# Optimization experiments

Measured on AMD Instinct MI355X. Metric: run time of the kernel, lower is better.

## Reference

```python
import jax, jax.numpy as jnp
import numpy as np

N = 50000   # nodes
E = 800000  # edges (avg degree 16)
IN, H, OUT = 128, 128, 64


def setup_inputs() -> dict:
    key = jax.random.key(0)
    ks = jax.random.split(key, 8)

    def w(k, shape):
        fan_in = shape[0]
        return (jax.random.normal(k, shape, jnp.float32) / np.float32(np.sqrt(fan_in)))

    x = jax.random.normal(ks[0], (N, IN), jnp.float32)
    edge_index = jax.random.randint(ks[1], (2, E), 0, N, jnp.int64)
    return {
        "x": x,
        "edge_index": edge_index,
        "W1": w(ks[2], (IN, H)), "b1": jnp.zeros((H,), jnp.float32),
        "W2": w(ks[3], (H, H)),  "b2": jnp.zeros((H,), jnp.float32),
        "W3": w(ks[4], (H, H)),  "b3": jnp.zeros((H,), jnp.float32),
        "Wd1": w(ks[5], (H, H)), "bd1": jnp.zeros((H,), jnp.float32),
        "Wd2": w(ks[6], (H, OUT)), "bd2": jnp.zeros((OUT,), jnp.float32),
    }


def _gcn_conv(x, src, dst, norm, W, b):
    # x: [N, Cin] -> linear transform, gather along edges, normalized scatter-add
    h = x @ W                                   # [N, Cout]
    msg = h[src] * norm[:, None]                # [E+N, Cout]
    out = jax.ops.segment_sum(msg, dst, num_segments=N)
    return out + b


def reference(x, edge_index, W1, b1, W2, b2, W3, b3, Wd1, bd1, Wd2, bd2):
    # Add self-loops (PyG GCNConv default) and compute symmetric normalization.
    loops = jnp.arange(N, dtype=edge_index.dtype)
    src = jnp.concatenate([edge_index[0], loops])   # [E+N]
    dst = jnp.concatenate([edge_index[1], loops])   # [E+N]
    deg = jax.ops.segment_sum(jnp.ones_like(dst, dtype=x.dtype), dst, num_segments=N)
    dinv = jnp.where(deg > 0, jax.lax.rsqrt(deg), jnp.zeros_like(deg))
    norm = dinv[src] * dinv[dst]                    # [E+N]

    h = jax.nn.relu(_gcn_conv(x, src, dst, norm, W1, b1))
    h = jax.nn.relu(_gcn_conv(h, src, dst, norm, W2, b2))
    h = jax.nn.relu(_gcn_conv(h, src, dst, norm, W3, b3))

    h = jax.nn.relu(h @ Wd1 + bd1)
    return jax.nn.sigmoid(h @ Wd2 + bd2)            # [N, OUT]
```

## Files before the change

kernel.cpp:

```cpp
#include <hip/hip_runtime.h>
#include <hip/hip_bf16.h>
#include <hip/hip_fp16.h>

#define N_NODES 50000
#define N_EDGES 800000
#define C_H 128
#define C_OUT 64
#define NBLK 196
#define TSTRIDE 136
#define E_PAD 950272

typedef __attribute__((ext_vector_type(8))) short bf16x8;
typedef __attribute__((ext_vector_type(4))) float f32x4;

static __device__ __forceinline__ float bf_lo(unsigned int u) { return __uint_as_float(u << 16); }
static __device__ __forceinline__ float bf_hi(unsigned int u) { return __uint_as_float(u & 0xffff0000u); }
static __device__ __forceinline__ unsigned short f2bf(float f) {
    __hip_bfloat16 h = __float2bfloat16(f);
    return *(unsigned short*)&h;
}
static __device__ __forceinline__ unsigned int pack2(float a, float b) {
    return (unsigned int)f2bf(a) | ((unsigned int)f2bf(b) << 16);
}
static __device__ __forceinline__ unsigned short f2h_bits(float f) {
    union { __half h; unsigned short u; } c; c.h = __float2half_rn(f); return c.u;
}
static __device__ __forceinline__ float h_bits2f(unsigned short u) {
    union { __half h; unsigned short u; } c; c.u = u; return __half2float(c.h);
}

__global__ void prep_kernel(const float* __restrict__ x, unsigned short* __restrict__ xb,
                            const int* __restrict__ dst, int* __restrict__ counts,
                            const float* __restrict__ W1, const float* __restrict__ W2,
                            const float* __restrict__ W3, const float* __restrict__ Wd1,
                            const float* __restrict__ Wd2,
                            unsigned short* __restrict__ P1, unsigned short* __restrict__ P2,
                            unsigned short* __restrict__ P3, unsigned short* __restrict__ Pd1,
                            unsigned short* __restrict__ Pd2) {
    int b = blockIdx.x;
    if (b < 6250) {
        int i = b * 256 + threadIdx.x;
        float4 v = *(const float4*)(x + (size_t)i * 4);
        ushort4 u;
        u.x = f2bf(v.x); u.y = f2bf(v.y); u.z = f2bf(v.z); u.w = f2bf(v.w);
        *(ushort4*)(xb + (size_t)i * 4) = u;
    } else if (b < 6250 + 3125) {
        int e = (b - 6250) * 256 + threadIdx.x;
        atomicAdd(&counts[dst[e]], 1);
    } else {
        int idx = (b - 9375) * 256 + threadIdx.x;
        if (idx < 4 * 16384) {
            int which = idx >> 14;
            int r = idx & 16383;
            const float* W = (which == 0) ? W1 : (which == 1) ? W2 : (which == 2) ? W3 : Wd1;
            unsigned short* P = (which == 0) ? P1 : (which == 1) ? P2 : (which == 2) ? P3 : Pd1;
            int j = r & 7, lane = (r >> 3) & 63, t = r >> 9;
            int nb = t & 7, kb = t >> 3;
            int k = kb * 32 + ((lane >> 4) << 3) + j;
            int n = nb * 16 + (lane & 15);
            P[r] = f2bf(W[(size_t)k * 128 + n]);
        } else {
            int r = idx - 65536;
            if (r < 8192) {
                int j = r & 7, lane = (r >> 3) & 63, t = r >> 9;
                int nb = t & 3, kb = t >> 2;
                int k = kb * 32 + ((lane >> 4) << 3) + j;
                int n = nb * 16 + (lane & 15);
                Pd2[r] = f2bf(Wd2[(size_t)k * 64 + n]);
            }
        }
    }
}

__global__ void __launch_bounds__(256) scan1_kernel(const int* __restrict__ counts,
                                                    int* __restrict__ eblk,
                                                    int* __restrict__ bsum,
                                                    float* __restrict__ dinv) {
    __shared__ int ws[4];
    int i = blockIdx.x * 256 + threadIdx.x;
    int v = (i < N_NODES) ? counts[i] : 0;
    if (i < N_NODES) dinv[i] = rsqrtf((float)v + 1.0f);
    int vp = (v + 3) & ~3;
    int lane = threadIdx.x & 63, w = threadIdx.x >> 6;
    int x = vp;
    #pragma unroll
    for (int off = 1; off < 64; off <<= 1) {
        int t = __shfl_up(x, off, 64);
        if (lane >= off) x += t;
    }
    if (lane == 63) ws[w] = x;
    __syncthreads();
    if (threadIdx.x == 0) {
        int run = 0;
        #pragma unroll
        for (int k = 0; k < 4; ++k) { int t = ws[k]; ws[k] = run; run += t; }
        bsum[blockIdx.x] = run;
    }
    __syncthreads();
    if (i < N_NODES) eblk[i] = x - vp + ws[w];
}

__global__ void __launch_bounds__(256) scan2_kernel(const int* __restrict__ bsum,
                                                    int* __restrict__ bo,
                                                    int* __restrict__ rowptr) {
    __shared__ int ws[4];
    int i = threadIdx.x;
    int v = (i < NBLK) ? bsum[i] : 0;
    int lane = i & 63, w = i >> 6;
    int x = v;
    #pragma unroll
    for (int off = 1; off < 64; off <<= 1) {
        int t = __shfl_up(x, off, 64);
        if (lane >= off) x += t;
    }
    if (lane == 63) ws[w] = x;
    __syncthreads();
    if (i == 0) {
        int run = 0;
        #pragma unroll
        for (int k = 0; k < 4; ++k) { int t = ws[k]; ws[k] = run; run += t; }
    }
    __syncthreads();
    int excl = x - v + ws[w];
    if (i < NBLK) bo[i] = excl;
    if (i == 255) rowptr[N_NODES] = excl + v;
}

__global__ void scan3_kernel(const int* __restrict__ eblk, const int* __restrict__ bo,
                             int* __restrict__ rowptr, int* __restrict__ cursor) {
    int i = blockIdx.x * 256 + threadIdx.x;
    if (i < N_NODES) {
        int r = eblk[i] + bo[blockIdx.x];
        rowptr[i] = r;
        cursor[i] = r;
    }
}

__global__ void csr_fill_kernel(const int* __restrict__ src, const int* __restrict__ dst,
                                const float* __restrict__ dinv,
                                int* __restrict__ cursor,
                                unsigned int* __restrict__ epay) {
    int e = blockIdx.x * 256 + threadIdx.x;
    if (e < N_EDGES) {
        int d = dst[e], s = src[e];
        int pos = atomicAdd(&cursor[d], 1);
        float nrm = dinv[s] * dinv[d];
        epay[pos] = (unsigned int)s | ((unsigned int)f2h_bits(nrm) << 16);
    }
}

template <bool FINAL>
__global__ void __launch_bounds__(256) fused_layer_kernel(
        const int* __restrict__ rowptr,
        const unsigned int* __restrict__ epay,
        const float* __restrict__ dinv,
        const unsigned short* __restrict__ hin,
        const unsigned short* __restrict__ Wp,
        const float* __restrict__ bias,
        const unsigned short* __restrict__ Wd1p,
        const float* __restrict__ bd1,
        const unsigned short* __restrict__ Wd2p,
        const float* __restrict__ bd2,
        unsigned short* __restrict__ out_b,
        float* __restrict__ out_f) {
    __shared__ unsigned short sG[16 * TSTRIDE];
    const int t = threadIdx.x;

    {
        int nl = t >> 4, c8 = (t & 15) << 3;
        int node = blockIdx.x * 16 + nl;
        float di = dinv[node], dii = di * di;
        uint4 raw = *(const uint4*)(hin + (size_t)node * C_H + c8);
        float a0 = bf_lo(raw.x) * dii, a1 = bf_hi(raw.x) * dii;
        float a2 = bf_lo(raw.y) * dii, a3 = bf_hi(raw.y) * dii;
        float a4 = bf_lo(raw.z) * dii, a5 = bf_hi(raw.z) * dii;
        float a6 = bf_lo(raw.w) * dii, a7 = bf_hi(raw.w) * dii;
        int beg = rowptr[node], end = rowptr[node + 1];
        for (int p = beg; p < end; p += 4) {
            uint4 ev = *(const uint4*)(epay + p);
            int   s0 = (int)(ev.x & 0xffffu); float n0 = h_bits2f((unsigned short)(ev.x >> 16));
            int   s1 = (int)(ev.y & 0xffffu); float n1 = h_bits2f((unsigned short)(ev.y >> 16));
            int   s2 = (int)(ev.z & 0xffffu); float n2 = h_bits2f((unsigned short)(ev.z >> 16));
            int   s3 = (int)(ev.w & 0xffffu); float n3 = h_bits2f((unsigned short)(ev.w >> 16));
            uint4 r0 = *(const uint4*)(hin + (size_t)s0 * C_H + c8);
            uint4 r1 = *(const uint4*)(hin + (size_t)s1 * C_H + c8);
            uint4 r2 = *(const uint4*)(hin + (size_t)s2 * C_H + c8);
            uint4 r3 = *(const uint4*)(hin + (size_t)s3 * C_H + c8);
            a0 = fmaf(bf_lo(r0.x), n0, a0); a1 = fmaf(bf_hi(r0.x), n0, a1);
            a2 = fmaf(bf_lo(r0.y), n0, a2); a3 = fmaf(bf_hi(r0.y), n0, a3);
            a4 = fmaf(bf_lo(r0.z), n0, a4); a5 = fmaf(bf_hi(r0.z), n0, a5);
            a6 = fmaf(bf_lo(r0.w), n0, a6); a7 = fmaf(bf_hi(r0.w), n0, a7);
            a0 = fmaf(bf_lo(r1.x), n1, a0); a1 = fmaf(bf_hi(r1.x), n1, a1);
            a2 = fmaf(bf_lo(r1.y), n1, a2); a3 = fmaf(bf_hi(r1.y), n1, a3);
            a4 = fmaf(bf_lo(r1.z), n1, a4); a5 = fmaf(bf_hi(r1.z), n1, a5);
            a6 = fmaf(bf_lo(r1.w), n1, a6); a7 = fmaf(bf_hi(r1.w), n1, a7);
            a0 = fmaf(bf_lo(r2.x), n2, a0); a1 = fmaf(bf_hi(r2.x), n2, a1);
            a2 = fmaf(bf_lo(r2.y), n2, a2); a3 = fmaf(bf_hi(r2.y), n2, a3);
            a4 = fmaf(bf_lo(r2.z), n2, a4); a5 = fmaf(bf_hi(r2.z), n2, a5);
            a6 = fmaf(bf_lo(r2.w), n2, a6); a7 = fmaf(bf_hi(r2.w), n2, a7);
            a0 = fmaf(bf_lo(r3.x), n3, a0); a1 = fmaf(bf_hi(r3.x), n3, a1);
            a2 = fmaf(bf_lo(r3.y), n3, a2); a3 = fmaf(bf_hi(r3.y), n3, a3);
            a4 = fmaf(bf_lo(r3.z), n3, a4); a5 = fmaf(bf_hi(r3.z), n3, a5);
            a6 = fmaf(bf_lo(r3.w), n3, a6); a7 = fmaf(bf_hi(r3.w), n3, a7);
        }
        uint4 o;
        o.x = pack2(a0, a1); o.y = pack2(a2, a3);
        o.z = pack2(a4, a5); o.w = pack2(a6, a7);
        *(uint4*)(sG + nl * TSTRIDE + c8) = o;
    }
    __syncthreads();

    const int lane = t & 63, wave = t >> 6, quad = lane >> 4, row = lane & 15;
    const int node = blockIdx.x * 16 + row;

    f32x4 acc0 = (f32x4){0.f, 0.f, 0.f, 0.f};
    f32x4 acc1 = (f32x4){0.f, 0.f, 0.f, 0.f};
    const int nb0 = 2 * wave, nb1 = 2 * wave + 1;
    #pragma unroll
    for (int kb = 0; kb < 4; ++kb) {
        bf16x8 hf = *(const bf16x8*)(sG + row * TSTRIDE + kb * 32 + quad * 8);
        bf16x8 wf0 = *(const bf16x8*)(Wp + ((size_t)(kb * 8 + nb0) * 64 + lane) * 8);
        bf16x8 wf1 = *(const bf16x8*)(Wp + ((size_t)(kb * 8 + nb1) * 64 + lane) * 8);
        acc0 = __builtin_amdgcn_mfma_f32_16x16x32_bf16(wf0, hf, acc0, 0, 0, 0);
        acc1 = __builtin_amdgcn_mfma_f32_16x16x32_bf16(wf1, hf, acc1, 0, 0, 0);
    }
    float4 ba0 = *(const float4*)(bias + nb0 * 16 + quad * 4);
    float4 ba1 = *(const float4*)(bias + nb1 * 16 + quad * 4);
    float v00 = fmaxf(acc0[0] + ba0.x, 0.f), v01 = fmaxf(acc0[1] + ba0.y, 0.f);
    float v02 = fmaxf(acc0[2] + ba0.z, 0.f), v03 = fmaxf(acc0[3] + ba0.w, 0.f);
    float v10 = fmaxf(acc1[0] + ba1.x, 0.f), v11 = fmaxf(acc1[1] + ba1.y, 0.f);
    float v12 = fmaxf(acc1[2] + ba1.z, 0.f), v13 = fmaxf(acc1[3] + ba1.w, 0.f);

    if (!FINAL) {
        uint2 o0, o1;
        o0.x = pack2(v00, v01); o0.y = pack2(v02, v03);
        o1.x = pack2(v10, v11); o1.y = pack2(v12, v13);
        *(uint2*)(out_b + (size_t)node * C_H + nb0 * 16 + quad * 4) = o0;
        *(uint2*)(out_b + (size_t)node * C_H + nb1 * 16 + quad * 4) = o1;
        return;
    }

    __syncthreads();
    {
        uint2 o0, o1;
        o0.x = pack2(v00, v01); o0.y = pack2(v02, v03);
        o1.x = pack2(v10, v11); o1.y = pack2(v12, v13);
        *(uint2*)(sG + row * TSTRIDE + nb0 * 16 + quad * 4) = o0;
        *(uint2*)(sG + row * TSTRIDE + nb1 * 16 + quad * 4) = o1;
    }
    __syncthreads();

    acc0 = (f32x4){0.f, 0.f, 0.f, 0.f};
    acc1 = (f32x4){0.f, 0.f, 0.f, 0.f};
    #pragma unroll
    for (int kb = 0; kb < 4; ++kb) {
        bf16x8 hf = *(const bf16x8*)(sG + row * TSTRIDE + kb * 32 + quad * 8);
        bf16x8 wf0 = *(const bf16x8*)(Wd1p + ((size_t)(kb * 8 + nb0) * 64 + lane) * 8);
        bf16x8 wf1 = *(const bf16x8*)(Wd1p + ((size_t)(kb * 8 + nb1) * 64 + lane) * 8);
        acc0 = __builtin_amdgcn_mfma_f32_16x16x32_bf16(wf0, hf, acc0, 0, 0, 0);
        acc1 = __builtin_amdgcn_mfma_f32_16x16x32_bf16(wf1, hf, acc1, 0, 0, 0);
    }
    ba0 = *(const float4*)(bd1 + nb0 * 16 + quad * 4);
    ba1 = *(const float4*)(bd1 + nb1 * 16 + quad * 4);
    v00 = fmaxf(acc0[0] + ba0.x, 0.f); v01 = fmaxf(acc0[1] + ba0.y, 0.f);
    v02 = fmaxf(acc0[2] + ba0.z, 0.f); v03 = fmaxf(acc0[3] + ba0.w, 0.f);
    v10 = fmaxf(acc1[0] + ba1.x, 0.f); v11 = fmaxf(acc1[1] + ba1.y, 0.f);
    v12 = fmaxf(acc1[2] + ba1.z, 0.f); v13 = fmaxf(acc1[3] + ba1.w, 0.f);
    __syncthreads();
    {
        uint2 o0, o1;
        o0.x = pack2(v00, v01); o0.y = pack2(v02, v03);
        o1.x = pack2(v10, v11); o1.y = pack2(v12, v13);
        *(uint2*)(sG + row * TSTRIDE + nb0 * 16 + quad * 4) = o0;
        *(uint2*)(sG + row * TSTRIDE + nb1 * 16 + quad * 4) = o1;
    }
    __syncthreads();

    f32x4 acc = (f32x4){0.f, 0.f, 0.f, 0.f};
    #pragma unroll
    for (int kb = 0; kb < 4; ++kb) {
        bf16x8 hf = *(const bf16x8*)(sG + row * TSTRIDE + kb * 32 + quad * 8);
        bf16x8 wf = *(const bf16x8*)(Wd2p + ((size_t)(kb * 4 + wave) * 64 + lane) * 8);
        acc = __builtin_amdgcn_mfma_f32_16x16x32_bf16(wf, hf, acc, 0, 0, 0);
    }
    int ch = wave * 16 + quad * 4;
    float4 b4 = *(const float4*)(bd2 + ch);
    float4 r;
    r.x = 1.f / (1.f + expf(-(acc[0] + b4.x)));
    r.y = 1.f / (1.f + expf(-(acc[1] + b4.y)));
    r.z = 1.f / (1.f + expf(-(acc[2] + b4.z)));
    r.w = 1.f / (1.f + expf(-(acc[3] + b4.w)));
    *(float4*)(out_f + (size_t)node * C_OUT + ch) = r;
}

extern "C" void kernel_launch(void* const* d_in, const int* in_sizes, int n_in,
                              void* d_out, int out_size, void* d_ws, size_t ws_size,
                              hipStream_t stream) {
    const float* x   = (const float*)d_in[0];
    const int*   ei  = (const int*)d_in[1];
    const float* W1  = (const float*)d_in[2];
    const float* b1  = (const float*)d_in[3];
    const float* W2  = (const float*)d_in[4];
    const float* b2  = (const float*)d_in[5];
    const float* W3  = (const float*)d_in[6];
    const float* b3  = (const float*)d_in[7];
    const float* Wd1 = (const float*)d_in[8];
    const float* bd1 = (const float*)d_in[9];
    const float* Wd2 = (const float*)d_in[10];
    const float* bd2 = (const float*)d_in[11];

    const int* src = ei;
    const int* dst = ei + N_EDGES;

    char* base = (char*)d_ws;
    size_t off = 0;
    auto alloc = [&](size_t bytes) { char* p = base + off; off += (bytes + 255) & ~size_t(255); return p; };
    int*            counts = (int*)alloc(50176 * 4);
    unsigned int*   epay   = (unsigned int*)alloc((size_t)E_PAD * 4);
    float*          dinv   = (float*)alloc(N_NODES * 4);
    int*            rowptr = (int*)alloc((N_NODES + 1) * 4);
    int*            cursor = (int*)alloc(N_NODES * 4);
    int*            eblk   = (int*)alloc(N_NODES * 4);
    int*            bsum   = (int*)alloc(256 * 4);
    int*            bo     = (int*)alloc(256 * 4);
    unsigned short* xb     = (unsigned short*)alloc((size_t)N_NODES * C_H * 2);
    unsigned short* bufA   = (unsigned short*)alloc((size_t)N_NODES * C_H * 2);
    unsigned short* bufB   = (unsigned short*)alloc((size_t)N_NODES * C_H * 2);
    unsigned short* P1     = (unsigned short*)alloc(128 * 128 * 2);
    unsigned short* P2     = (unsigned short*)alloc(128 * 128 * 2);
    unsigned short* P3     = (unsigned short*)alloc(128 * 128 * 2);
    unsigned short* Pd1    = (unsigned short*)alloc(128 * 128 * 2);
    unsigned short* Pd2    = (unsigned short*)alloc(128 * 64 * 2);

    const int T = 256;
    dim3 blk(T);
    dim3 gN((N_NODES + T - 1) / T);
    dim3 gE((N_EDGES + T - 1) / T);
    dim3 gPrep(6250 + 3125 + 288);
    dim3 gFused(N_NODES / 16);

    hipMemsetAsync(counts, 0, 50176 * 4 + (size_t)E_PAD * 4, stream);
    prep_kernel<<<gPrep, blk, 0, stream>>>(x, xb, dst, counts,
                                           W1, W2, W3, Wd1, Wd2, P1, P2, P3, Pd1, Pd2);
    scan1_kernel<<<gN, blk, 0, stream>>>(counts, eblk, bsum, dinv);
    scan2_kernel<<<1, blk, 0, stream>>>(bsum, bo, rowptr);
    scan3_kernel<<<gN, blk, 0, stream>>>(eblk, bo, rowptr, cursor);
    csr_fill_kernel<<<gE, blk, 0, stream>>>(src, dst, dinv, cursor, epay);

    fused_layer_kernel<false><<<gFused, blk, 0, stream>>>(
        rowptr, epay, dinv, xb, P1, b1, nullptr, nullptr, nullptr, nullptr, bufA, nullptr);
    fused_layer_kernel<false><<<gFused, blk, 0, stream>>>(
        rowptr, epay, dinv, bufA, P2, b2, nullptr, nullptr, nullptr, nullptr, bufB, nullptr);
    fused_layer_kernel<true><<<gFused, blk, 0, stream>>>(
        rowptr, epay, dinv, bufB, P3, b3, Pd1, bd1, Pd2, bd2, nullptr, (float*)d_out);
}
```

Measured before the change: 280.9 us.

## Record edge ranks during counting, drop cursor atomics, widen gather unroll

The degree-counting pass now stores the return value of its atomicAdd as a per-edge rank. The CSR fill then computes each slot as rowptr[dst] + rank, with no second pass of atomics on a cursor array. Zeroing of the padded edge payload moves from the memset into extra prep blocks. The gather loop now processes 8 edges per iteration, issuing eight independent row loads before the FMAs for more memory-level parallelism, with a 4-edge tail step. The cost is an extra 3.2 MB rank array written and read, plus higher register pressure in the fused layer kernel.

```diff
diff --git a/kernel.cpp b/kernel.cpp
--- a/kernel.cpp
+++ b/kernel.cpp
@@ -31,12 +31,14 @@
 
 __global__ void prep_kernel(const float* __restrict__ x, unsigned short* __restrict__ xb,
                             const int* __restrict__ dst, int* __restrict__ counts,
+                            int* __restrict__ rank,
                             const float* __restrict__ W1, const float* __restrict__ W2,
                             const float* __restrict__ W3, const float* __restrict__ Wd1,
                             const float* __restrict__ Wd2,
                             unsigned short* __restrict__ P1, unsigned short* __restrict__ P2,
                             unsigned short* __restrict__ P3, unsigned short* __restrict__ Pd1,
-                            unsigned short* __restrict__ Pd2) {
+                            unsigned short* __restrict__ Pd2,
+                            unsigned int* __restrict__ epay) {
     int b = blockIdx.x;
     if (b < 6250) {
         int i = b * 256 + threadIdx.x;
@@ -44,10 +46,10 @@
         ushort4 u;
         u.x = f2bf(v.x); u.y = f2bf(v.y); u.z = f2bf(v.z); u.w = f2bf(v.w);
         *(ushort4*)(xb + (size_t)i * 4) = u;
-    } else if (b < 6250 + 3125) {
+    } else if (b < 9375) {
         int e = (b - 6250) * 256 + threadIdx.x;
-        atomicAdd(&counts[dst[e]], 1);
-    } else {
+        rank[e] = atomicAdd(&counts[dst[e]], 1);
+    } else if (b < 9663) {
         int idx = (b - 9375) * 256 + threadIdx.x;
         if (idx < 4 * 16384) {
             int which = idx >> 14;
@@ -69,6 +71,9 @@
                 Pd2[r] = f2bf(Wd2[(size_t)k * 64 + n]);
             }
         }
+    } else {
+        int i = (b - 9663) * 256 + threadIdx.x;
+        *(uint4*)(epay + (size_t)i * 4) = make_uint4(0, 0, 0, 0);
     }
 }
 
@@ -127,23 +132,19 @@
 }
 
 __global__ void scan3_kernel(const int* __restrict__ eblk, const int* __restrict__ bo,
-                             int* __restrict__ rowptr, int* __restrict__ cursor) {
+                             int* __restrict__ rowptr) {
     int i = blockIdx.x * 256 + threadIdx.x;
-    if (i < N_NODES) {
-        int r = eblk[i] + bo[blockIdx.x];
-        rowptr[i] = r;
-        cursor[i] = r;
-    }
+    if (i < N_NODES) rowptr[i] = eblk[i] + bo[blockIdx.x];
 }
 
 __global__ void csr_fill_kernel(const int* __restrict__ src, const int* __restrict__ dst,
                                 const float* __restrict__ dinv,
-                                int* __restrict__ cursor,
+                                const int* __restrict__ rowptr, const int* __restrict__ rank,
                                 unsigned int* __restrict__ epay) {
     int e = blockIdx.x * 256 + threadIdx.x;
     if (e < N_EDGES) {
         int d = dst[e], s = src[e];
-        int pos = atomicAdd(&cursor[d], 1);
+        int pos = rowptr[d] + rank[e];
         float nrm = dinv[s] * dinv[d];
         epay[pos] = (unsigned int)s | ((unsigned int)f2h_bits(nrm) << 16);
     }
@@ -176,32 +177,39 @@
         float a4 = bf_lo(raw.z) * dii, a5 = bf_hi(raw.z) * dii;
         float a6 = bf_lo(raw.w) * dii, a7 = bf_hi(raw.w) * dii;
         int beg = rowptr[node], end = rowptr[node + 1];
-        for (int p = beg; p < end; p += 4) {
+        int p = beg;
+        for (; p + 8 <= end; p += 8) {
+            uint4 ev0 = *(const uint4*)(epay + p);
+            uint4 ev1 = *(const uint4*)(epay + p + 4);
+            unsigned int ee[8] = {ev0.x, ev0.y, ev0.z, ev0.w, ev1.x, ev1.y, ev1.z, ev1.w};
+            uint4 rv[8];
+            #pragma unroll
+            for (int j = 0; j < 8; ++j)
+                rv[j] = *(const uint4*)(hin + (size_t)(ee[j] & 0xffffu) * C_H + c8);
+            #pragma unroll
+            for (int j = 0; j < 8; ++j) {
+                float nm = h_bits2f((unsigned short)(ee[j] >> 16));
+                a0 = fmaf(bf_lo(rv[j].x), nm, a0); a1 = fmaf(bf_hi(rv[j].x), nm, a1);
+                a2 = fmaf(bf_lo(rv[j].y), nm, a2); a3 = fmaf(bf_hi(rv[j].y), nm, a3);
+                a4 = fmaf(bf_lo(rv[j].z), nm, a4); a5 = fmaf(bf_hi(rv[j].z), nm, a5);
+                a6 = fmaf(bf_lo(rv[j].w), nm, a6); a7 = fmaf(bf_hi(rv[j].w), nm, a7);
+            }
+        }
+        if (p < end) {
             uint4 ev = *(const uint4*)(epay + p);
-            int   s0 = (int)(ev.x & 0xffffu); float n0 = h_bits2f((unsigned short)(ev.x >> 16));
-            int   s1 = (int)(ev.y & 0xffffu); float n1 = h_bits2f((unsigned short)(ev.y >> 16));
-            int   s2 = (int)(ev.z & 0xffffu); float n2 = h_bits2f((unsigned short)(ev.z >> 16));
-            int   s3 = (int)(ev.w & 0xffffu); float n3 = h_bits2f((unsigned short)(ev.w >> 16));
-            uint4 r0 = *(const uint4*)(hin + (size_t)s0 * C_H + c8);
-            uint4 r1 = *(const uint4*)(hin + (size_t)s1 * C_H + c8);
-            uint4 r2 = *(const uint4*)(hin + (size_t)s2 * C_H + c8);
-            uint4 r3 = *(const uint4*)(hin + (size_t)s3 * C_H + c8);
-            a0 = fmaf(bf_lo(r0.x), n0, a0); a1 = fmaf(bf_hi(r0.x), n0, a1);
-            a2 = fmaf(bf_lo(r0.y), n0, a2); a3 = fmaf(bf_hi(r0.y), n0, a3);
-            a4 = fmaf(bf_lo(r0.z), n0, a4); a5 = fmaf(bf_hi(r0.z), n0, a5);
-            a6 = fmaf(bf_lo(r0.w), n0, a6); a7 = fmaf(bf_hi(r0.w), n0, a7);
-            a0 = fmaf(bf_lo(r1.x), n1, a0); a1 = fmaf(bf_hi(r1.x), n1, a1);
-            a2 = fmaf(bf_lo(r1.y), n1, a2); a3 = fmaf(bf_hi(r1.y), n1, a3);
-            a4 = fmaf(bf_lo(r1.z), n1, a4); a5 = fmaf(bf_hi(r1.z), n1, a5);
-            a6 = fmaf(bf_lo(r1.w), n1, a6); a7 = fmaf(bf_hi(r1.w), n1, a7);
-            a0 = fmaf(bf_lo(r2.x), n2, a0); a1 = fmaf(bf_hi(r2.x), n2, a1);
-            a2 = fmaf(bf_lo(r2.y), n2, a2); a3 = fmaf(bf_hi(r2.y), n2, a3);
-            a4 = fmaf(bf_lo(r2.z), n2, a4); a5 = fmaf(bf_hi(r2.z), n2, a5);
-            a6 = fmaf(bf_lo(r2.w), n2, a6); a7 = fmaf(bf_hi(r2.w), n2, a7);
-            a0 = fmaf(bf_lo(r3.x), n3, a0); a1 = fmaf(bf_hi(r3.x), n3, a1);
-            a2 = fmaf(bf_lo(r3.y), n3, a2); a3 = fmaf(bf_hi(r3.y), n3, a3);
-            a4 = fmaf(bf_lo(r3.z), n3, a4); a5 = fmaf(bf_hi(r3.z), n3, a5);
-            a6 = fmaf(bf_lo(r3.w), n3, a6); a7 = fmaf(bf_hi(r3.w), n3, a7);
+            unsigned int ee[4] = {ev.x, ev.y, ev.z, ev.w};
+            uint4 rv[4];
+            #pragma unroll
+            for (int j = 0; j < 4; ++j)
+                rv[j] = *(const uint4*)(hin + (size_t)(ee[j] & 0xffffu) * C_H + c8);
+            #pragma unroll
+            for (int j = 0; j < 4; ++j) {
+                float nm = h_bits2f((unsigned short)(ee[j] >> 16));
+                a0 = fmaf(bf_lo(rv[j].x), nm, a0); a1 = fmaf(bf_hi(rv[j].x), nm, a1);
+                a2 = fmaf(bf_lo(rv[j].y), nm, a2); a3 = fmaf(bf_hi(rv[j].y), nm, a3);
+                a4 = fmaf(bf_lo(rv[j].z), nm, a4); a5 = fmaf(bf_hi(rv[j].z), nm, a5);
+                a6 = fmaf(bf_lo(rv[j].w), nm, a6); a7 = fmaf(bf_hi(rv[j].w), nm, a7);
+            }
         }
         uint4 o;
         o.x = pack2(a0, a1); o.y = pack2(a2, a3);
@@ -317,9 +325,9 @@
     auto alloc = [&](size_t bytes) { char* p = base + off; off += (bytes + 255) & ~size_t(255); return p; };
     int*            counts = (int*)alloc(50176 * 4);
     unsigned int*   epay   = (unsigned int*)alloc((size_t)E_PAD * 4);
+    int*            rank   = (int*)alloc((size_t)N_EDGES * 4);
     float*          dinv   = (float*)alloc(N_NODES * 4);
     int*            rowptr = (int*)alloc((N_NODES + 1) * 4);
-    int*            cursor = (int*)alloc(N_NODES * 4);
     int*            eblk   = (int*)alloc(N_NODES * 4);
     int*            bsum   = (int*)alloc(256 * 4);
     int*            bo     = (int*)alloc(256 * 4);
@@ -336,16 +344,17 @@
     dim3 blk(T);
     dim3 gN((N_NODES + T - 1) / T);
     dim3 gE((N_EDGES + T - 1) / T);
-    dim3 gPrep(6250 + 3125 + 288);
+    dim3 gPrep(6250 + 3125 + 288 + 928);
     dim3 gFused(N_NODES / 16);
 
-    hipMemsetAsync(counts, 0, 50176 * 4 + (size_t)E_PAD * 4, stream);
-    prep_kernel<<<gPrep, blk, 0, stream>>>(x, xb, dst, counts,
-                                           W1, W2, W3, Wd1, Wd2, P1, P2, P3, Pd1, Pd2);
+    hipMemsetAsync(counts, 0, 50176 * 4, stream);
+    prep_kernel<<<gPrep, blk, 0, stream>>>(x, xb, dst, counts, rank,
+                                           W1, W2, W3, Wd1, Wd2,
+                                           P1, P2, P3, Pd1, Pd2, epay);
     scan1_kernel<<<gN, blk, 0, stream>>>(counts, eblk, bsum, dinv);
     scan2_kernel<<<1, blk, 0, stream>>>(bsum, bo, rowptr);
-    scan3_kernel<<<gN, blk, 0, stream>>>(eblk, bo, rowptr, cursor);
-    csr_fill_kernel<<<gE, blk, 0, stream>>>(src, dst, dinv, cursor, epay);
+    scan3_kernel<<<gN, blk, 0, stream>>>(eblk, bo, rowptr);
+    csr_fill_kernel<<<gE, blk, 0, stream>>>(src, dst, dinv, rowptr, rank, epay);
 
     fused_layer_kernel<false><<<gFused, blk, 0, stream>>>(
         rowptr, epay, dinv, xb, P1, b1, nullptr, nullptr, nullptr, nullptr, bufA, nullptr);
```

Measured after the change: 258.7 us. 1.09x faster.
